# Optimization experiments

Measured on AMD Instinct MI355X. Metric: run time of the kernel, lower is better.

Reference implementation:

```python
import jax, jax.numpy as jnp
import numpy as np

B, T = 32, 512
TOK, DIR = 26, 26
EMB, H, L, OUT = 512, 1024, 2, 26
LN_EPS = 1e-5


def setup_inputs() -> dict:
    key = jax.random.key(0)
    ks = jax.random.split(key, 16)
    s = lambda fan_in: 1.0 / np.sqrt(fan_in)
    inp = {
        "t": jax.random.normal(ks[0], (B, T, TOK), jnp.float32),
        "c": jax.random.normal(ks[1], (B, T, DIR), jnp.float32),
        # SharedLinear projections (no bias)
        "W_tok": jax.random.uniform(ks[2], (EMB // 2, TOK), jnp.float32, -s(TOK), s(TOK)),
        "W_coord": jax.random.uniform(ks[3], (EMB // 2, DIR), jnp.float32, -s(DIR), s(DIR)),
        # embedding Linear(EMB -> H) + ReLU
        "W_emb": jax.random.uniform(ks[4], (H, EMB), jnp.float32, -s(EMB), s(EMB)),
        "b_emb": jax.random.uniform(ks[5], (H,), jnp.float32, -s(EMB), s(EMB)),
        # GRU weights stacked over layers: (L, 3H, H) / (L, 3H)
        "W_ih": jax.random.uniform(ks[6], (L, 3 * H, H), jnp.float32, -s(H), s(H)),
        "W_hh": jax.random.uniform(ks[7], (L, 3 * H, H), jnp.float32, -s(H), s(H)),
        "b_ih": jax.random.uniform(ks[8], (L, 3 * H), jnp.float32, -s(H), s(H)),
        "b_hh": jax.random.uniform(ks[9], (L, 3 * H), jnp.float32, -s(H), s(H)),
        # LayerNorm(H)
        "gamma": jnp.ones((H,), jnp.float32),
        "beta": jnp.zeros((H,), jnp.float32),
        # fc_proj SharedLinear(H -> H), readout SharedLinear(H -> OUT)
        "W_fc": jax.random.uniform(ks[10], (H, H), jnp.float32, -s(H), s(H)),
        "W_ro": jax.random.uniform(ks[11], (OUT, H), jnp.float32, -s(H), s(H)),
    }
    return inp


def _gru_unroll(emb, W_ih, W_hh, b_ih, b_hh):
    """emb: (B,T,H). Returns top_out (B,T,H), acts/z/r/n each (L,B,T,H)."""
    Bv = emb.shape[0]
    h0 = jnp.zeros((L, Bv, H), emb.dtype)

    def step(h, x_t):  # h: (L,B,H), x_t: (B,H)
        x = x_t
        hs, zs, rs, ns = [], [], [], []
        for l in range(L):
            h_prev = h[l]
            i_lin = x @ W_ih[l].T + b_ih[l]          # (B, 3H)
            h_lin = h_prev @ W_hh[l].T + b_hh[l]     # (B, 3H)
            i_r, i_z, i_n = jnp.split(i_lin, 3, axis=1)
            h_r, h_z, h_n = jnp.split(h_lin, 3, axis=1)
            r = jax.nn.sigmoid(i_r + h_r)
            z = jax.nn.sigmoid(i_z + h_z)
            n = jnp.tanh(i_n + r * h_n)
            h_new = n + z * (h_prev - n)
            hs.append(h_new); zs.append(z); rs.append(r); ns.append(n)
            x = h_new
        h_next = jnp.stack(hs)
        return h_next, (h_next, jnp.stack(zs), jnp.stack(rs), jnp.stack(ns))

    _, (acts, zg, rg, ng) = jax.lax.scan(step, h0, jnp.swapaxes(emb, 0, 1))
    # (T,L,B,H) -> (L,B,T,H)
    perm = (1, 2, 0, 3)
    acts, zg, rg, ng = (jnp.transpose(a, perm) for a in (acts, zg, rg, ng))
    top_out = acts[-1]
    return top_out, acts, zg, rg, ng


def reference(t, c, W_tok, W_coord, W_emb, b_emb, W_ih, W_hh, b_ih, b_hh,
              gamma, beta, W_fc, W_ro):
    proj = jnp.concatenate([t @ W_tok.T, c @ W_coord.T], axis=2)  # (B,T,EMB)
    emb = jax.nn.relu(proj @ W_emb.T + b_emb)                     # (B,T,H)
    top_out, acts, zg, rg, ng = _gru_unroll(emb, W_ih, W_hh, b_ih, b_hh)
    mu = jnp.mean(top_out, axis=-1, keepdims=True)
    var = jnp.var(top_out, axis=-1, keepdims=True)
    normed = (top_out - mu) * jax.lax.rsqrt(var + LN_EPS) * gamma + beta
    fc_out = jax.nn.relu(normed @ W_fc.T)
    output = fc_out @ W_ro.T                                      # readout transpose=True == plain no-bias linear
    return output, acts, zg, rg, ng
```

## Files before the change

### kernel.cpp

```cpp
#include <hip/hip_runtime.h>

#define B_ 32
#define T_ 512
#define H_ 1024
#define TOK_ 26
#define EMB_ 512
#define OUT_ 26

__global__ void k_fuse_w(const float* __restrict__ W_emb, const float* __restrict__ W_tok,
                         const float* __restrict__ W_coord, float* __restrict__ Wt,
                         float* __restrict__ Wc) {
    int idx = blockIdx.x * 256 + threadIdx.x;
    if (idx >= 2 * H_ * TOK_) return;
    int which = idx >= H_ * TOK_;
    int rem = idx - which * (H_ * TOK_);
    int h = rem / TOK_;
    int k = rem - h * TOK_;
    const float* Wsel = which ? W_coord : W_tok;
    const float* we = W_emb + (size_t)h * EMB_ + which * 256;
    float acc = 0.f;
#pragma unroll 8
    for (int e = 0; e < 256; ++e) acc += we[e] * Wsel[e * TOK_ + k];
    (which ? Wc : Wt)[h * TOK_ + k] = acc;
}

__global__ void k_embed(const float* __restrict__ t_in, const float* __restrict__ c_in,
                        const float* __restrict__ Wt, const float* __restrict__ Wc,
                        const float* __restrict__ b_emb, float* __restrict__ emb) {
    int row = blockIdx.x;
    int tid = threadIdx.x;
    __shared__ float tv[TOK_], cv[TOK_];
    if (tid < TOK_) tv[tid] = t_in[(size_t)row * TOK_ + tid];
    else if (tid < 2 * TOK_) cv[tid - TOK_] = c_in[(size_t)row * TOK_ + (tid - TOK_)];
    __syncthreads();
#pragma unroll
    for (int i = 0; i < 4; ++i) {
        int h = tid + i * 256;
        float acc = b_emb[h];
        const float* wt = Wt + h * TOK_;
        const float* wc = Wc + h * TOK_;
#pragma unroll
        for (int k = 0; k < TOK_; ++k) acc += tv[k] * wt[k] + cv[k] * wc[k];
        emb[(size_t)row * H_ + h] = fmaxf(acc, 0.f);
    }
}

__global__ __launch_bounds__(512) void k_gru(
    const float* __restrict__ x_base, long long x_stride,
    const float* __restrict__ h_prev, float* __restrict__ h_new,
    const float* __restrict__ W_ih, const float* __restrict__ W_hh,
    const float* __restrict__ b_ih, const float* __restrict__ b_hh,
    float* __restrict__ o_act, float* __restrict__ o_z,
    float* __restrict__ o_r, float* __restrict__ o_n, int t) {
    __shared__ float xt[32][132];
    __shared__ float ht[32][132];
    __shared__ float part[3][4][32][3];
    int tid = threadIdx.x;
    int b = tid & 31;
    int dd = (tid >> 5) & 3;
    int ks = tid >> 7;
    int d = blockIdx.x * 4 + dd;
    int mat = ks >> 1;
    int khalf = ks & 1;
    const float* Wb = mat ? W_hh : W_ih;
    const float* Wr = Wb + (size_t)d * H_;
    const float* Wz = Wb + (size_t)(H_ + d) * H_;
    const float* Wn = Wb + (size_t)(2 * H_ + d) * H_;
    float ar = 0.f, az = 0.f, an = 0.f;
    int cbase = khalf * 64;
    for (int it = 0; it < 8; ++it) {
#pragma unroll
        for (int j = 0; j < 4; ++j) {
            int i4 = tid + j * 512;
            int sel = i4 >> 10;
            int slot = i4 & 1023;
            int bb = slot >> 5;
            int cc = (slot & 31) << 2;
            int gc = (cc < 64) ? (it * 64 + cc) : (512 + it * 64 + (cc - 64));
            const float* src = sel ? (h_prev + (size_t)bb * H_)
                                   : (x_base + (size_t)bb * x_stride);
            float4 v = *(const float4*)(src + gc);
            float* dst = sel ? &ht[bb][cc] : &xt[bb][cc];
            *(float4*)dst = v;
        }
        __syncthreads();
        const float(*tile)[132] = mat ? ht : xt;
        int koff = khalf * 512 + it * 64;
#pragma unroll
        for (int k = 0; k < 64; k += 4) {
            float4 v = *(const float4*)&tile[b][cbase + k];
            float4 wr = *(const float4*)(Wr + koff + k);
            float4 wz = *(const float4*)(Wz + koff + k);
            float4 wn = *(const float4*)(Wn + koff + k);
            ar += v.x * wr.x + v.y * wr.y + v.z * wr.z + v.w * wr.w;
            az += v.x * wz.x + v.y * wz.y + v.z * wz.z + v.w * wz.w;
            an += v.x * wn.x + v.y * wn.y + v.z * wn.z + v.w * wn.w;
        }
        __syncthreads();
    }
    if (ks != 0) {
        part[ks - 1][dd][b][0] = ar;
        part[ks - 1][dd][b][1] = az;
        part[ks - 1][dd][b][2] = an;
    }
    __syncthreads();
    if (ks == 0) {
        float rpre = ar + part[0][dd][b][0] + part[1][dd][b][0] + part[2][dd][b][0]
                   + b_ih[d] + b_hh[d];
        float zpre = az + part[0][dd][b][1] + part[1][dd][b][1] + part[2][dd][b][1]
                   + b_ih[H_ + d] + b_hh[H_ + d];
        float ni = an + part[0][dd][b][2] + b_ih[2 * H_ + d];
        float nh = part[1][dd][b][2] + part[2][dd][b][2] + b_hh[2 * H_ + d];
        float r = 1.f / (1.f + expf(-rpre));
        float z = 1.f / (1.f + expf(-zpre));
        float n = tanhf(ni + r * nh);
        float hp = h_prev[b * H_ + d];
        float hn = n + z * (hp - n);
        h_new[b * H_ + d] = hn;
        size_t o = ((size_t)b * T_ + t) * H_ + d;
        o_act[o] = hn;
        o_z[o] = z;
        o_r[o] = r;
        o_n[o] = n;
    }
}

__global__ void k_lnstats(const float* __restrict__ top, float* __restrict__ stats) {
    int row = blockIdx.x;
    int tid = threadIdx.x;
    float4 v = *(const float4*)(top + (size_t)row * H_ + tid * 4);
    float s = v.x + v.y + v.z + v.w;
    float ss = v.x * v.x + v.y * v.y + v.z * v.z + v.w * v.w;
    for (int off = 32; off; off >>= 1) {
        s += __shfl_down(s, off, 64);
        ss += __shfl_down(ss, off, 64);
    }
    __shared__ float sb[4], ssb[4];
    int w = tid >> 6;
    if ((tid & 63) == 0) { sb[w] = s; ssb[w] = ss; }
    __syncthreads();
    if (tid == 0) {
        float S = sb[0] + sb[1] + sb[2] + sb[3];
        float SS = ssb[0] + ssb[1] + ssb[2] + ssb[3];
        float mu = S * (1.f / H_);
        float var = SS * (1.f / H_) - mu * mu;
        stats[row * 2] = mu;
        stats[row * 2 + 1] = rsqrtf(var + 1e-5f);
    }
}

__global__ __launch_bounds__(256) void k_fc(const float* __restrict__ top,
                                            const float* __restrict__ stats,
                                            const float* __restrict__ gamma,
                                            const float* __restrict__ beta,
                                            const float* __restrict__ W_fc,
                                            float* __restrict__ fc_out) {
    __shared__ float At[64][17];
    __shared__ float Bt[64][17];
    __shared__ float mu_s[64], rs_s[64];
    int tid = threadIdx.x;
    int m0 = blockIdx.x * 64;
    int j0 = blockIdx.y * 64;
    if (tid < 64) {
        mu_s[tid] = stats[(size_t)(m0 + tid) * 2];
        rs_s[tid] = stats[(size_t)(m0 + tid) * 2 + 1];
    }
    __syncthreads();
    int ty = tid >> 4, tx = tid & 15;
    float acc[4][4] = {};
    for (int kt = 0; kt < H_; kt += 16) {
#pragma unroll
        for (int i = 0; i < 4; ++i) {
            int idx = tid + i * 256;
            int r = idx >> 4, k = idx & 15;
            float raw = top[(size_t)(m0 + r) * H_ + kt + k];
            At[r][k] = (raw - mu_s[r]) * rs_s[r] * gamma[kt + k] + beta[kt + k];
            Bt[r][k] = W_fc[(size_t)(j0 + r) * H_ + kt + k];
        }
        __syncthreads();
#pragma unroll
        for (int k = 0; k < 16; ++k) {
            float a0 = At[ty * 4 + 0][k], a1 = At[ty * 4 + 1][k];
            float a2 = At[ty * 4 + 2][k], a3 = At[ty * 4 + 3][k];
            float b0 = Bt[tx * 4 + 0][k], b1 = Bt[tx * 4 + 1][k];
            float b2 = Bt[tx * 4 + 2][k], b3 = Bt[tx * 4 + 3][k];
            acc[0][0] += a0 * b0; acc[0][1] += a0 * b1; acc[0][2] += a0 * b2; acc[0][3] += a0 * b3;
            acc[1][0] += a1 * b0; acc[1][1] += a1 * b1; acc[1][2] += a1 * b2; acc[1][3] += a1 * b3;
            acc[2][0] += a2 * b0; acc[2][1] += a2 * b1; acc[2][2] += a2 * b2; acc[2][3] += a2 * b3;
            acc[3][0] += a3 * b0; acc[3][1] += a3 * b1; acc[3][2] += a3 * b2; acc[3][3] += a3 * b3;
        }
        __syncthreads();
    }
#pragma unroll
    for (int i = 0; i < 4; ++i)
#pragma unroll
        for (int j = 0; j < 4; ++j)
            fc_out[(size_t)(m0 + ty * 4 + i) * H_ + j0 + tx * 4 + j] = fmaxf(acc[i][j], 0.f);
}

__global__ void k_ro(const float* __restrict__ fc_out, const float* __restrict__ W_ro,
                     float* __restrict__ out) {
    int row = blockIdx.x;
    int tid = threadIdx.x;
    __shared__ float xrow[H_];
    *(float4*)&xrow[tid * 4] = *(const float4*)(fc_out + (size_t)row * H_ + tid * 4);
    __syncthreads();
    int o = tid >> 3, ks = tid & 7;
    float acc = 0.f;
    if (o < OUT_) {
        const float* w = W_ro + (size_t)o * H_ + ks * 128;
        const float* xs = xrow + ks * 128;
#pragma unroll 16
        for (int k = 0; k < 128; ++k) {
            int idx = (k + 4 * ks) & 127;
            acc += xs[idx] * w[idx];
        }
    }
    __shared__ float red[OUT_][8];
    if (o < OUT_) red[o][ks] = acc;
    __syncthreads();
    if (tid < OUT_) {
        float s = 0.f;
#pragma unroll
        for (int i = 0; i < 8; ++i) s += red[tid][i];
        out[(size_t)row * OUT_ + tid] = s;
    }
}

extern "C" void kernel_launch(void* const* d_in, const int* in_sizes, int n_in,
                              void* d_out, int out_size, void* d_ws, size_t ws_size,
                              hipStream_t stream) {
    (void)in_sizes; (void)n_in; (void)out_size; (void)ws_size;
    const float* t_in    = (const float*)d_in[0];
    const float* c_in    = (const float*)d_in[1];
    const float* W_tok   = (const float*)d_in[2];
    const float* W_coord = (const float*)d_in[3];
    const float* W_emb   = (const float*)d_in[4];
    const float* b_emb   = (const float*)d_in[5];
    const float* W_ih    = (const float*)d_in[6];
    const float* W_hh    = (const float*)d_in[7];
    const float* b_ih    = (const float*)d_in[8];
    const float* b_hh    = (const float*)d_in[9];
    const float* gamma   = (const float*)d_in[10];
    const float* beta    = (const float*)d_in[11];
    const float* W_fc    = (const float*)d_in[12];
    const float* W_ro    = (const float*)d_in[13];

    float* out = (float*)d_out;
    const size_t NOUT0 = (size_t)B_ * T_ * OUT_;
    const size_t NBTH  = (size_t)B_ * T_ * H_;
    const size_t NLBTH = 2 * NBTH;
    float* o_acts = out + NOUT0;
    float* o_z = o_acts + NLBTH;
    float* o_r = o_z + NLBTH;
    float* o_n = o_r + NLBTH;

    float* ws = (float*)d_ws;
    float* fc_out = ws;
    float* stats  = ws + 16777216;
    float* hbuf   = stats + 32768;
    float* Wt     = hbuf + 4 * B_ * H_;
    float* Wc     = Wt + H_ * TOK_;

    float* emb = o_n + NBTH;

    hipMemsetAsync(hbuf, 0, (size_t)2 * B_ * H_ * sizeof(float), stream);

    k_fuse_w<<<(2 * H_ * TOK_ + 255) / 256, 256, 0, stream>>>(W_emb, W_tok, W_coord, Wt, Wc);
    k_embed<<<B_ * T_, 256, 0, stream>>>(t_in, c_in, Wt, Wc, b_emb, emb);

    for (int t = 0; t < T_; ++t) {
        int rp = t & 1, wp = rp ^ 1;
        float* h0r = hbuf + (rp * 2 + 0) * (B_ * H_);
        float* h0w = hbuf + (wp * 2 + 0) * (B_ * H_);
        float* h1r = hbuf + (rp * 2 + 1) * (B_ * H_);
        float* h1w = hbuf + (wp * 2 + 1) * (B_ * H_);
        k_gru<<<256, 512, 0, stream>>>(emb + (size_t)t * H_, (long long)(T_ * H_),
                                       h0r, h0w, W_ih, W_hh, b_ih, b_hh,
                                       o_acts, o_z, o_r, o_n, t);
        k_gru<<<256, 512, 0, stream>>>(h0w, (long long)H_,
                                       h1r, h1w,
                                       W_ih + (size_t)3 * H_ * H_, W_hh + (size_t)3 * H_ * H_,
                                       b_ih + 3 * H_, b_hh + 3 * H_,
                                       o_acts + NBTH, o_z + NBTH, o_r + NBTH, o_n + NBTH, t);
    }

    k_lnstats<<<B_ * T_, 256, 0, stream>>>(o_acts + NBTH, stats);
    k_fc<<<dim3((B_ * T_) / 64, H_ / 64), 256, 0, stream>>>(o_acts + NBTH, stats, gamma, beta,
                                                            W_fc, fc_out);
    k_ro<<<B_ * T_, 256, 0, stream>>>(fc_out, W_ro, out);
}
```

Measured before the change: 42.72 ms.

## Replace per-step GRU launches with persistent kernel and hoisted input GEMM

The layer-0 input projection is hoisted out of the recurrence into one large tiled GEMM, written into spare output planes. The 1024 per-timestep launches are replaced by a single persistent kernel that keeps each block's slice of the recurrent weights resident in LDS (36 rows x 1024). It pipelines layer 1 one step behind layer 0 and syncs steps with a software grid barrier. This removes launch overhead and repeated weight streaming from global memory. The cost is the ~144KB LDS footprint, a spin barrier with a timeout that assumes all 256 blocks are co-resident, and reuse of output buffers as scratch.

```diff
diff --git a/kernel.cpp b/kernel.cpp
--- a/kernel.cpp
+++ b/kernel.cpp
@@ -6,6 +6,8 @@
 #define TOK_ 26
 #define EMB_ 512
 #define OUT_ 26
+#define BH_ (B_ * H_)
+#define NBTH_ ((size_t)B_ * T_ * H_)
 
 __global__ void k_fuse_w(const float* __restrict__ W_emb, const float* __restrict__ W_tok,
                          const float* __restrict__ W_coord, float* __restrict__ Wt,
@@ -45,83 +47,253 @@
     }
 }
 
-__global__ __launch_bounds__(512) void k_gru(
-    const float* __restrict__ x_base, long long x_stride,
-    const float* __restrict__ h_prev, float* __restrict__ h_new,
+__global__ __launch_bounds__(256) void k_i0(const float* __restrict__ A,
+                                            const float* __restrict__ W,
+                                            const float* __restrict__ bias,
+                                            float* __restrict__ p0, float* __restrict__ p1,
+                                            float* __restrict__ p2) {
+    __shared__ float As[32][132];
+    __shared__ float Bs[32][132];
+    int tid = threadIdx.x;
+    int m0 = blockIdx.x * 128, n0 = blockIdx.y * 128;
+    int ty = tid >> 4, tx = tid & 15;
+    float acc[8][8] = {};
+    for (int k0 = 0; k0 < 1024; k0 += 32) {
+#pragma unroll
+        for (int p = 0; p < 4; ++p) {
+            int idx = tid + p * 256;
+            int r = idx >> 3, c = idx & 7;
+            float4 va = *(const float4*)(A + (size_t)(m0 + r) * 1024 + k0 + c * 4);
+            float4 vb = *(const float4*)(W + (size_t)(n0 + r) * 1024 + k0 + c * 4);
+            As[c * 4 + 0][r] = va.x; As[c * 4 + 1][r] = va.y;
+            As[c * 4 + 2][r] = va.z; As[c * 4 + 3][r] = va.w;
+            Bs[c * 4 + 0][r] = vb.x; Bs[c * 4 + 1][r] = vb.y;
+            Bs[c * 4 + 2][r] = vb.z; Bs[c * 4 + 3][r] = vb.w;
+        }
+        __syncthreads();
+#pragma unroll 8
+        for (int kk = 0; kk < 32; ++kk) {
+            float af[8], bf[8];
+#pragma unroll
+            for (int i = 0; i < 8; ++i) af[i] = As[kk][ty * 8 + i];
+#pragma unroll
+            for (int i = 0; i < 8; ++i) bf[i] = Bs[kk][tx * 8 + i];
+#pragma unroll
+            for (int i = 0; i < 8; ++i)
+#pragma unroll
+                for (int j = 0; j < 8; ++j) acc[i][j] += af[i] * bf[j];
+        }
+        __syncthreads();
+    }
+    int g = n0 >> 10;
+    float* plane = g == 0 ? p0 : (g == 1 ? p1 : p2);
+    int dbase = (n0 & 1023) + tx * 8;
+    float bs[8];
+#pragma unroll
+    for (int j = 0; j < 8; ++j) bs[j] = bias[n0 + tx * 8 + j];
+#pragma unroll
+    for (int i = 0; i < 8; ++i) {
+        int m = m0 + ty * 8 + i;
+#pragma unroll
+        for (int j = 0; j < 8; ++j)
+            plane[(size_t)m * 1024 + dbase + j] = acc[i][j] + bs[j];
+    }
+}
+
+__device__ __forceinline__ void grid_barrier(unsigned* cnt, unsigned* gen, unsigned nblk) {
+    __syncthreads();
+    if (threadIdx.x == 0) {
+        __threadfence();
+        unsigned g = __hip_atomic_load(gen, __ATOMIC_RELAXED, __HIP_MEMORY_SCOPE_AGENT);
+        unsigned arrived =
+            __hip_atomic_fetch_add(cnt, 1u, __ATOMIC_ACQ_REL, __HIP_MEMORY_SCOPE_AGENT);
+        if (arrived == nblk - 1) {
+            __hip_atomic_store(cnt, 0u, __ATOMIC_RELAXED, __HIP_MEMORY_SCOPE_AGENT);
+            __hip_atomic_store(gen, g + 1u, __ATOMIC_RELEASE, __HIP_MEMORY_SCOPE_AGENT);
+        } else {
+            long long t0 = __builtin_amdgcn_s_memrealtime();
+            while (__hip_atomic_load(gen, __ATOMIC_ACQUIRE, __HIP_MEMORY_SCOPE_AGENT) == g) {
+                __builtin_amdgcn_s_sleep(8);
+                if (__builtin_amdgcn_s_memrealtime() - t0 > 100000000LL) break;
+            }
+        }
+        __threadfence();
+    }
+    __syncthreads();
+}
+
+__global__ __launch_bounds__(512, 2) void k_gru_persist(
+    const float* __restrict__ i0r, const float* __restrict__ i0z, const float* __restrict__ i0n,
     const float* __restrict__ W_ih, const float* __restrict__ W_hh,
     const float* __restrict__ b_ih, const float* __restrict__ b_hh,
-    float* __restrict__ o_act, float* __restrict__ o_z,
-    float* __restrict__ o_r, float* __restrict__ o_n, int t) {
-    __shared__ float xt[32][132];
-    __shared__ float ht[32][132];
-    __shared__ float part[3][4][32][3];
-    int tid = threadIdx.x;
-    int b = tid & 31;
-    int dd = (tid >> 5) & 3;
-    int ks = tid >> 7;
-    int d = blockIdx.x * 4 + dd;
-    int mat = ks >> 1;
-    int khalf = ks & 1;
-    const float* Wb = mat ? W_hh : W_ih;
-    const float* Wr = Wb + (size_t)d * H_;
-    const float* Wz = Wb + (size_t)(H_ + d) * H_;
-    const float* Wn = Wb + (size_t)(2 * H_ + d) * H_;
-    float ar = 0.f, az = 0.f, an = 0.f;
-    int cbase = khalf * 64;
-    for (int it = 0; it < 8; ++it) {
-#pragma unroll
-        for (int j = 0; j < 4; ++j) {
-            int i4 = tid + j * 512;
-            int sel = i4 >> 10;
-            int slot = i4 & 1023;
-            int bb = slot >> 5;
-            int cc = (slot & 31) << 2;
-            int gc = (cc < 64) ? (it * 64 + cc) : (512 + it * 64 + (cc - 64));
-            const float* src = sel ? (h_prev + (size_t)bb * H_)
-                                   : (x_base + (size_t)bb * x_stride);
-            float4 v = *(const float4*)(src + gc);
-            float* dst = sel ? &ht[bb][cc] : &xt[bb][cc];
-            *(float4*)dst = v;
+    float* __restrict__ hbuf,
+    float* __restrict__ o_acts, float* __restrict__ o_z,
+    float* __restrict__ o_r, float* __restrict__ o_n,
+    unsigned* __restrict__ bar) {
+    __shared__ float lw[36][1024];
+    __shared__ float sums[36][32];
+    int bid = blockIdx.x;
+    int tid = threadIdx.x;
+    unsigned* bcnt = bar;
+    unsigned* bgen = bar + 1;
+
+    {
+        const float* W1i = W_ih + (size_t)3 * H_ * H_;
+        const float* W1h = W_hh + (size_t)3 * H_ * H_;
+        for (int idx = tid; idx < 36 * 256; idx += 512) {
+            int r = idx >> 8, c4 = (idx & 255) << 2;
+            const float* src;
+            if (r < 12) {
+                src = W_hh + ((size_t)(r >> 2) * H_ + bid * 4 + (r & 3)) * H_;
+            } else if (r < 24) {
+                int rr = r - 12;
+                src = W1i + ((size_t)(rr >> 2) * H_ + bid * 4 + (rr & 3)) * H_;
+            } else {
+                int rr = r - 24;
+                src = W1h + ((size_t)(rr >> 2) * H_ + bid * 4 + (rr & 3)) * H_;
+            }
+            *(float4*)&lw[r][c4] = *(const float4*)(src + c4);
+        }
+    }
+
+    int grp = tid >> 8;
+    int u = tid & 255;
+    int ks = u & 31, bg = (u >> 5) & 3, rg = u >> 7;
+    int qj = tid & 3, qb = (tid >> 2) & 31, qd = bid * 4 + (tid & 3);
+
+    float bA_r = 0, bA_z = 0, bA_n = 0;
+    float bB_ir = 0, bB_iz = 0, bB_in = 0, bB_hr = 0, bB_hz = 0, bB_hn = 0;
+    if (grp == 0) {
+        if (tid < 128) {
+            bA_r = b_hh[qd]; bA_z = b_hh[H_ + qd]; bA_n = b_hh[2 * H_ + qd];
+        }
+    } else if (tid < 384) {
+        const float* bi1 = b_ih + 3 * H_;
+        const float* bh1 = b_hh + 3 * H_;
+        bB_ir = bi1[qd]; bB_iz = bi1[H_ + qd]; bB_in = bi1[2 * H_ + qd];
+        bB_hr = bh1[qd]; bB_hz = bh1[H_ + qd]; bB_hn = bh1[2 * H_ + qd];
+    }
+    __syncthreads();
+
+    for (int s = 0; s <= T_; ++s) {
+        int par = s & 1;
+        const float* h0p = hbuf + (par * 2 + 0) * BH_;
+        const float* h1p = hbuf + (par * 2 + 1) * BH_;
+        float* h0n_ = hbuf + ((par ^ 1) * 2 + 0) * BH_;
+        float* h1n_ = hbuf + ((par ^ 1) * 2 + 1) * BH_;
+
+        float pir = 0, piz = 0, pin = 0, php = 0;
+        if (grp == 0) {
+            if (tid < 128 && s < T_) {
+                size_t o = ((size_t)qb * T_ + s) * H_ + qd;
+                pir = i0r[o]; piz = i0z[o]; pin = i0n[o];
+                php = h0p[qb * H_ + qd];
+            }
+        } else {
+            if (tid < 384 && s >= 1) php = h1p[qb * H_ + qd];
+        }
+
+        if (grp == 0) {
+            const float* hb = h0p + (size_t)(bg * 8) * H_ + ks * 4;
+            const float* wb = &lw[rg * 6][0] + ks * 4;
+            float acc[6][8];
+#pragma unroll
+            for (int i = 0; i < 6; ++i)
+#pragma unroll
+                for (int b2 = 0; b2 < 8; ++b2) acc[i][b2] = 0.f;
+#pragma unroll 2
+            for (int kq = 0; kq < 8; ++kq) {
+                float4 hh[8];
+#pragma unroll
+                for (int b2 = 0; b2 < 8; ++b2)
+                    hh[b2] = *(const float4*)(hb + (size_t)b2 * H_ + kq * 128);
+#pragma unroll
+                for (int i = 0; i < 6; ++i) {
+                    float4 wv = *(const float4*)(wb + i * 1024 + kq * 128);
+#pragma unroll
+                    for (int b2 = 0; b2 < 8; ++b2)
+                        acc[i][b2] += wv.x * hh[b2].x + wv.y * hh[b2].y +
+                                      wv.z * hh[b2].z + wv.w * hh[b2].w;
+                }
+            }
+#pragma unroll
+            for (int i = 0; i < 6; ++i)
+#pragma unroll
+                for (int b2 = 0; b2 < 8; ++b2) {
+                    float v = acc[i][b2];
+                    v += __shfl_xor(v, 1);  v += __shfl_xor(v, 2);
+                    v += __shfl_xor(v, 4);  v += __shfl_xor(v, 8);
+                    v += __shfl_xor(v, 16);
+                    if (ks == 0) sums[rg * 6 + i][bg * 8 + b2] = v;
+                }
+        } else {
+            const float* hsrc = rg ? h1p : h0p;
+            int R0 = 12 + rg * 12;
+            const float* hb = hsrc + (size_t)(bg * 8) * H_ + ks * 4;
+            const float* wb = &lw[R0][0] + ks * 4;
+            float acc[12][8];
+#pragma unroll
+            for (int i = 0; i < 12; ++i)
+#pragma unroll
+                for (int b2 = 0; b2 < 8; ++b2) acc[i][b2] = 0.f;
+#pragma unroll 2
+            for (int kq = 0; kq < 8; ++kq) {
+                float4 hh[8];
+#pragma unroll
+                for (int b2 = 0; b2 < 8; ++b2)
+                    hh[b2] = *(const float4*)(hb + (size_t)b2 * H_ + kq * 128);
+#pragma unroll
+                for (int i = 0; i < 12; ++i) {
+                    float4 wv = *(const float4*)(wb + i * 1024 + kq * 128);
+#pragma unroll
+                    for (int b2 = 0; b2 < 8; ++b2)
+                        acc[i][b2] += wv.x * hh[b2].x + wv.y * hh[b2].y +
+                                      wv.z * hh[b2].z + wv.w * hh[b2].w;
+                }
+            }
+#pragma unroll
+            for (int i = 0; i < 12; ++i)
+#pragma unroll
+                for (int b2 = 0; b2 < 8; ++b2) {
+                    float v = acc[i][b2];
+                    v += __shfl_xor(v, 1);  v += __shfl_xor(v, 2);
+                    v += __shfl_xor(v, 4);  v += __shfl_xor(v, 8);
+                    v += __shfl_xor(v, 16);
+                    if (ks == 0) sums[R0 + i][bg * 8 + b2] = v;
+                }
         }
         __syncthreads();
-        const float(*tile)[132] = mat ? ht : xt;
-        int koff = khalf * 512 + it * 64;
-#pragma unroll
-        for (int k = 0; k < 64; k += 4) {
-            float4 v = *(const float4*)&tile[b][cbase + k];
-            float4 wr = *(const float4*)(Wr + koff + k);
-            float4 wz = *(const float4*)(Wz + koff + k);
-            float4 wn = *(const float4*)(Wn + koff + k);
-            ar += v.x * wr.x + v.y * wr.y + v.z * wr.z + v.w * wr.w;
-            az += v.x * wz.x + v.y * wz.y + v.z * wz.z + v.w * wz.w;
-            an += v.x * wn.x + v.y * wn.y + v.z * wn.z + v.w * wn.w;
-        }
-        __syncthreads();
-    }
-    if (ks != 0) {
-        part[ks - 1][dd][b][0] = ar;
-        part[ks - 1][dd][b][1] = az;
-        part[ks - 1][dd][b][2] = an;
-    }
-    __syncthreads();
-    if (ks == 0) {
-        float rpre = ar + part[0][dd][b][0] + part[1][dd][b][0] + part[2][dd][b][0]
-                   + b_ih[d] + b_hh[d];
-        float zpre = az + part[0][dd][b][1] + part[1][dd][b][1] + part[2][dd][b][1]
-                   + b_ih[H_ + d] + b_hh[H_ + d];
-        float ni = an + part[0][dd][b][2] + b_ih[2 * H_ + d];
-        float nh = part[1][dd][b][2] + part[2][dd][b][2] + b_hh[2 * H_ + d];
-        float r = 1.f / (1.f + expf(-rpre));
-        float z = 1.f / (1.f + expf(-zpre));
-        float n = tanhf(ni + r * nh);
-        float hp = h_prev[b * H_ + d];
-        float hn = n + z * (hp - n);
-        h_new[b * H_ + d] = hn;
-        size_t o = ((size_t)b * T_ + t) * H_ + d;
-        o_act[o] = hn;
-        o_z[o] = z;
-        o_r[o] = r;
-        o_n[o] = n;
+
+        if (grp == 0) {
+            if (tid < 128 && s < T_) {
+                float hr = sums[qj][qb], hz = sums[4 + qj][qb], hn = sums[8 + qj][qb];
+                float r = 1.f / (1.f + expf(-(pir + hr + bA_r)));
+                float z = 1.f / (1.f + expf(-(piz + hz + bA_z)));
+                float n = tanhf(pin + r * (hn + bA_n));
+                float hnew = n + z * (php - n);
+                h0n_[qb * H_ + qd] = hnew;
+                size_t oo = ((size_t)qb * T_ + s) * H_ + qd;
+                o_acts[oo] = hnew; o_z[oo] = z; o_r[oo] = r; o_n[oo] = n;
+            }
+        } else {
+            if (tid < 384 && s >= 1) {
+                int t2 = s - 1;
+                float ir = sums[12 + qj][qb] + bB_ir;
+                float iz = sums[16 + qj][qb] + bB_iz;
+                float in_ = sums[20 + qj][qb] + bB_in;
+                float hr = sums[24 + qj][qb] + bB_hr;
+                float hz = sums[28 + qj][qb] + bB_hz;
+                float hn = sums[32 + qj][qb] + bB_hn;
+                float r = 1.f / (1.f + expf(-(ir + hr)));
+                float z = 1.f / (1.f + expf(-(iz + hz)));
+                float n = tanhf(in_ + r * hn);
+                float hnew = n + z * (php - n);
+                h1n_[qb * H_ + qd] = hnew;
+                size_t oo = NBTH_ + ((size_t)qb * T_ + t2) * H_ + qd;
+                o_acts[oo] = hnew; o_z[oo] = z; o_r[oo] = r; o_n[oo] = n;
+            }
+        }
+        if (s < T_) grid_barrier(bcnt, bgen, 256u);
     }
 }
 
@@ -257,33 +429,26 @@
 
     float* ws = (float*)d_ws;
     float* fc_out = ws;
+    float* emb    = ws;
     float* stats  = ws + 16777216;
     float* hbuf   = stats + 32768;
     float* Wt     = hbuf + 4 * B_ * H_;
     float* Wc     = Wt + H_ * TOK_;
-
-    float* emb = o_n + NBTH;
-
-    hipMemsetAsync(hbuf, 0, (size_t)2 * B_ * H_ * sizeof(float), stream);
+    unsigned* bar = (unsigned*)(Wc + H_ * TOK_);
+
+    float* i0r = o_z + NBTH;
+    float* i0z = o_r + NBTH;
+    float* i0n = o_n + NBTH;
+
+    hipMemsetAsync(hbuf, 0, (size_t)4 * B_ * H_ * sizeof(float), stream);
+    hipMemsetAsync(bar, 0, 2 * sizeof(unsigned), stream);
 
     k_fuse_w<<<(2 * H_ * TOK_ + 255) / 256, 256, 0, stream>>>(W_emb, W_tok, W_coord, Wt, Wc);
     k_embed<<<B_ * T_, 256, 0, stream>>>(t_in, c_in, Wt, Wc, b_emb, emb);
-
-    for (int t = 0; t < T_; ++t) {
-        int rp = t & 1, wp = rp ^ 1;
-        float* h0r = hbuf + (rp * 2 + 0) * (B_ * H_);
-        float* h0w = hbuf + (wp * 2 + 0) * (B_ * H_);
-        float* h1r = hbuf + (rp * 2 + 1) * (B_ * H_);
-        float* h1w = hbuf + (wp * 2 + 1) * (B_ * H_);
-        k_gru<<<256, 512, 0, stream>>>(emb + (size_t)t * H_, (long long)(T_ * H_),
-                                       h0r, h0w, W_ih, W_hh, b_ih, b_hh,
-                                       o_acts, o_z, o_r, o_n, t);
-        k_gru<<<256, 512, 0, stream>>>(h0w, (long long)H_,
-                                       h1r, h1w,
-                                       W_ih + (size_t)3 * H_ * H_, W_hh + (size_t)3 * H_ * H_,
-                                       b_ih + 3 * H_, b_hh + 3 * H_,
-                                       o_acts + NBTH, o_z + NBTH, o_r + NBTH, o_n + NBTH, t);
-    }
+    k_i0<<<dim3(128, 24), 256, 0, stream>>>(emb, W_ih, b_ih, i0r, i0z, i0n);
+
+    k_gru_persist<<<256, 512, 0, stream>>>(i0r, i0z, i0n, W_ih, W_hh, b_ih, b_hh,
+                                           hbuf, o_acts, o_z, o_r, o_n, bar);
 
     k_lnstats<<<B_ * T_, 256, 0, stream>>>(o_acts + NBTH, stats);
     k_fc<<<dim3((B_ * T_) / 64, H_ / 64), 256, 0, stream>>>(o_acts + NBTH, stats, gamma, beta,
```

Result: faster. 41.17 ms (-3.6%).
